# Optimization experiments

Hardware: AMD Instinct MI355X
Metric: run time of the kernel (lower is better)

## Reference

```python
import jax, jax.numpy as jnp
import numpy as np
from functools import partial

DIM = 1024
LIGHT_HID = 512   # dim * 0.5
HEAVY_HID = 4096  # dim * 4
NUM_HEAVY = 1024
N_ITERS = 50
K_ROUTE = 8.0
EPS = 0.1


def rms_norm(x, gamma):
    # F.normalize(x, dim=-1) * sqrt(dim) * gamma
    norm = jnp.linalg.norm(x, axis=-1, keepdims=True)
    normed = x / jnp.maximum(norm, 1e-12)
    return normed * (x.shape[-1] ** 0.5) * gamma


def ffn(x, gamma, w1, b1, w2, b2):
    h = rms_norm(x, gamma)
    h = jax.nn.gelu(h @ w1 + b1, approximate=False)
    return h @ w2 + b2


def coor_descent_route(x, routing_token, num_tokens):
    # s: [b, n]
    s = jnp.einsum('bnd,d->bn', x, routing_token)
    constant = EPS * jnp.log(jnp.asarray(K_ROUTE, dtype=s.dtype))
    b0 = -jax.nn.relu(s)
    a0 = jnp.zeros((s.shape[0], 1), dtype=s.dtype)

    def step(carry, _):
        a_prev, b = carry
        a = constant - EPS * jax.nn.logsumexp((s + b) / EPS, axis=-1, keepdims=True)
        b = -jax.nn.relu(s + a)
        return (a, b), None

    (a, b), _ = jax.lax.scan(step, (a0, b0), None, length=N_ITERS)
    scores = jnp.exp((s + a + b) / EPS)
    sel_scores, sel_idx = jax.lax.top_k(scores, num_tokens)
    # straight-through: value -> 1.0, gradient -> d(sel_scores)
    sel_scores = sel_scores + jax.lax.stop_gradient(1.0 - sel_scores)
    return sel_scores, sel_idx


def setup_inputs() -> dict:
    key = jax.random.key(0)
    ks = jax.random.split(key, 12)
    def lin(k, fan_in, fan_out):
        lim = 1.0 / np.sqrt(fan_in)
        kw, kb = jax.random.split(k)
        w = jax.random.uniform(kw, (fan_in, fan_out), jnp.float32, -lim, lim)
        b = jax.random.uniform(kb, (fan_out,), jnp.float32, -lim, lim)
        return w, b
    x = jax.random.normal(ks[0], (4, 8192, DIM), jnp.float32)
    routing_token = jax.random.normal(ks[1], (DIM,), jnp.float32)
    gamma_light = jnp.ones((DIM,), jnp.float32)
    w1_l, b1_l = lin(ks[2], DIM, LIGHT_HID)
    w2_l, b2_l = lin(ks[3], LIGHT_HID, DIM)
    gamma_heavy = jnp.ones((DIM,), jnp.float32)
    w1_h, b1_h = lin(ks[4], DIM, HEAVY_HID)
    w2_h, b2_h = lin(ks[5], HEAVY_HID, DIM)
    return dict(x=x, routing_token=routing_token,
                gamma_light=gamma_light, w1_light=w1_l, b1_light=b1_l,
                w2_light=w2_l, b2_light=b2_l,
                gamma_heavy=gamma_heavy, w1_heavy=w1_h, b1_heavy=b1_h,
                w2_heavy=w2_h, b2_heavy=b2_h)


def reference(x, routing_token, gamma_light, w1_light, b1_light, w2_light, b2_light,
              gamma_heavy, w1_heavy, b1_heavy, w2_heavy, b2_heavy):
    bsz = x.shape[0]
    light_out = ffn(x, gamma_light, w1_light, b1_light, w2_light, b2_light)
    sel_scores, sel_idx = coor_descent_route(x, routing_token, NUM_HEAVY)
    batch_range = jnp.arange(bsz)[:, None]           # [b, 1]
    routed = x[batch_range, sel_idx]                 # [b, k, d]
    routed_out = ffn(routed, gamma_heavy, w1_heavy, b1_heavy, w2_heavy, b2_heavy)
    routed_out = routed_out * sel_scores[..., None]
    heavy_out = jnp.zeros_like(x).at[batch_range, sel_idx].set(routed_out)
    return light_out + heavy_out
```

## Files before the change

### kernel.cpp

```cpp
#include <hip/hip_runtime.h>
#include <math.h>

#define TOKS   32768
#define NSEQ   8192
#define BATCH  4
#define DIMD   1024
#define LHID   512
#define HHID   4096
#define NHEAVY 1024

typedef __attribute__((ext_vector_type(8))) short bf16x8;
typedef __attribute__((ext_vector_type(4))) float f32x4;
typedef __attribute__((ext_vector_type(8))) unsigned short u16x8;
typedef __attribute__((ext_vector_type(4))) unsigned short u16x4;

__device__ __forceinline__ unsigned short bf16rne(float f) {
    unsigned u = __float_as_uint(f);
    return (unsigned short)((u + 0x7FFFu + ((u >> 16) & 1u)) >> 16);
}
__device__ __forceinline__ float gelu_f(float v) {
    return 0.5f * v * (1.0f + erff(v * 0.7071067811865476f));
}
__device__ __forceinline__ void gload_lds16(const unsigned short* g, unsigned short* l) {
#if defined(__HIP_DEVICE_COMPILE__)
    __builtin_amdgcn_global_load_lds((const __attribute__((address_space(1))) void*)g,
                                     (__attribute__((address_space(3))) void*)l,
                                     16, 0, 0);
#endif
}

__global__ __launch_bounds__(256) void k_rowscale(const float* __restrict__ x,
                                                  const float* __restrict__ rt,
                                                  const float* __restrict__ gamma,
                                                  float* __restrict__ s,
                                                  float* __restrict__ invr,
                                                  unsigned short* __restrict__ xl) {
    int wid = threadIdx.x >> 6, lane = threadIdx.x & 63;
    int row = blockIdx.x * 4 + wid;
    const float4* xr  = (const float4*)(x + (size_t)row * DIMD);
    const float4* rt4 = (const float4*)rt;
    const float4* g4  = (const float4*)gamma;
    float4 v[4];
    float dot = 0.f, ss = 0.f;
#pragma unroll
    for (int i = 0; i < 4; i++) {
        v[i] = xr[lane + 64 * i];
        float4 r = rt4[lane + 64 * i];
        dot += v[i].x * r.x + v[i].y * r.y + v[i].z * r.z + v[i].w * r.w;
        ss  += v[i].x * v[i].x + v[i].y * v[i].y + v[i].z * v[i].z + v[i].w * v[i].w;
    }
#pragma unroll
    for (int o = 32; o > 0; o >>= 1) {
        dot += __shfl_xor(dot, o);
        ss  += __shfl_xor(ss, o);
    }
    float iv = 32.0f / fmaxf(sqrtf(ss), 1e-12f);
    if (lane == 0) { s[row] = dot; invr[row] = iv; }
#pragma unroll
    for (int i = 0; i < 4; i++) {
        float4 g = g4[lane + 64 * i];
        u16x4 o;
        o[0] = bf16rne(v[i].x * iv * g.x);
        o[1] = bf16rne(v[i].y * iv * g.y);
        o[2] = bf16rne(v[i].z * iv * g.z);
        o[3] = bf16rne(v[i].w * iv * g.w);
        *(u16x4*)(xl + (size_t)row * DIMD + (lane + 64 * i) * 4) = o;
    }
}

__global__ __launch_bounds__(256) void k_rowstats(const float* __restrict__ x,
                                                  const float* __restrict__ rt,
                                                  float* __restrict__ s,
                                                  float* __restrict__ invr) {
    int wid = threadIdx.x >> 6, lane = threadIdx.x & 63;
    int row = blockIdx.x * 4 + wid;
    const float4* xr  = (const float4*)(x + (size_t)row * DIMD);
    const float4* rt4 = (const float4*)rt;
    float dot = 0.f, ss = 0.f;
#pragma unroll
    for (int i = 0; i < 4; i++) {
        float4 v = xr[lane + 64 * i];
        float4 r = rt4[lane + 64 * i];
        dot += v.x * r.x + v.y * r.y + v.z * r.z + v.w * r.w;
        ss  += v.x * v.x + v.y * v.y + v.z * v.z + v.w * v.w;
    }
#pragma unroll
    for (int o = 32; o > 0; o >>= 1) {
        dot += __shfl_down(dot, o);
        ss  += __shfl_down(ss, o);
    }
    if (lane == 0) {
        s[row] = dot;
        invr[row] = 32.0f / fmaxf(sqrtf(ss), 1e-12f);
    }
}

__global__ __launch_bounds__(1024) void k_routesel(const float* __restrict__ s_g,
                                                   int* __restrict__ rowmap) {
    int b = blockIdx.x, tid = threadIdx.x;
    int lane = tid & 63, wid = tid >> 6;
    __shared__ float red[2][16];
    __shared__ int wsum[16];
    __shared__ int ws2[16];
    __shared__ int PC[2];
    __shared__ int slot;
    __shared__ unsigned long long kk_[NSEQ];
    const float* sb = s_g + b * NSEQ;
    float sv[8];
    float smax = -3.4e38f;
#pragma unroll
    for (int i = 0; i < 8; i++) { sv[i] = sb[tid + 1024 * i]; smax = fmaxf(smax, sv[i]); }
#pragma unroll
    for (int o = 32; o > 0; o >>= 1) smax = fmaxf(smax, __shfl_xor(smax, o));
    if (lane == 0) red[0][wid] = smax;
    __syncthreads();
    float smaxAll = -3.4e38f;
    for (int w = 0; w < 16; w++) smaxAll = fmaxf(smaxAll, red[0][w]);
    __syncthreads();

    const float cst = 0.1f * logf(8.0f);
    float a = 0.0f;
    for (int it = 0; it < 50; it++) {
        float tau = -a;
        float M = fminf(smaxAll, tau);
        float p = 0.0f;
#pragma unroll
        for (int i = 0; i < 8; i++) p += expf((fminf(sv[i], tau) - M) * 10.0f);
#pragma unroll
        for (int o = 32; o > 0; o >>= 1) p += __shfl_xor(p, o);
        if (lane == 0) red[it & 1][wid] = p;
        __syncthreads();
        float S = 0.0f;
        for (int w = 0; w < 16; w++) S += red[it & 1][w];
        a = cst - M - 0.1f * logf(S);
        __syncthreads();
    }
    float sc[8];
    int p = 0, c1 = 0;
#pragma unroll
    for (int i = 0; i < 8; i++) {
        sc[i] = expf(fminf(sv[i] + a, 0.0f) * 10.0f);
        p  += (sc[i] > 0.0f) ? 1 : 0;
        c1 += (sc[i] == 1.0f) ? 1 : 0;
    }
    {
        int pp = p, cc = c1;
#pragma unroll
        for (int o = 32; o > 0; o >>= 1) {
            pp += __shfl_xor(pp, o);
            cc += __shfl_xor(cc, o);
        }
        if (lane == 0) { wsum[wid] = pp; ws2[wid] = cc; }
        __syncthreads();
        if (tid == 0) {
            int sp = 0, sC = 0;
            for (int w = 0; w < 16; w++) { sp += wsum[w]; sC += ws2[w]; }
            PC[0] = sp; PC[1] = sC;
        }
        __syncthreads();
    }
    int P = PC[0], C1 = PC[1];
    __syncthreads();

    if (C1 >= NHEAVY) {
        __shared__ unsigned char fl[NSEQ];
#pragma unroll
        for (int i = 0; i < 8; i++) fl[tid + 1024 * i] = (sc[i] == 1.0f) ? 1 : 0;
        __syncthreads();
        int zc = 0;
        unsigned char f[8];
#pragma unroll
        for (int j = 0; j < 8; j++) { f[j] = fl[tid * 8 + j]; zc += f[j]; }
        int inc = zc;
        for (int o = 1; o < 64; o <<= 1) {
            int t = __shfl_up(inc, o);
            if (lane >= o) inc += t;
        }
        if (lane == 63) wsum[wid] = inc;
        __syncthreads();
        if (tid == 0) {
            int acc = 0;
            for (int w = 0; w < 16; w++) { int t = wsum[w]; wsum[w] = acc; acc += t; }
        }
        __syncthreads();
        int rank = wsum[wid] + (inc - zc);
#pragma unroll
        for (int j = 0; j < 8; j++) {
            if (f[j]) {
                if (rank < NHEAVY) rowmap[b * NHEAVY + rank] = b * NSEQ + tid * 8 + j;
                rank++;
            }
        }
    } else if (P <= NHEAVY) {
        __shared__ unsigned char fl[NSEQ];
#pragma unroll
        for (int i = 0; i < 8; i++) fl[tid + 1024 * i] = (sc[i] > 0.0f) ? 1 : 0;
        __syncthreads();
        unsigned char pos[8]; int zc = 0;
#pragma unroll
        for (int j = 0; j < 8; j++) { pos[j] = fl[tid * 8 + j]; zc += pos[j] ? 0 : 1; }
        int inc = zc;
        for (int o = 1; o < 64; o <<= 1) {
            int t = __shfl_up(inc, o);
            if (lane >= o) inc += t;
        }
        if (lane == 63) wsum[wid] = inc;
        if (tid == 0) slot = 0;
        __syncthreads();
        if (tid == 0) {
            int acc = 0;
            for (int w = 0; w < 16; w++) { int t = wsum[w]; wsum[w] = acc; acc += t; }
        }
        __syncthreads();
        int zr = wsum[wid] + (inc - zc);
        int Z = NHEAVY - P;
#pragma unroll
        for (int j = 0; j < 8; j++) {
            int n = tid * 8 + j;
            bool sel;
            if (pos[j]) sel = true;
            else { sel = (zr < Z); zr += 1; }
            if (sel) {
                int sl = atomicAdd(&slot, 1);
                rowmap[b * NHEAVY + sl] = b * NSEQ + n;
            }
        }
    } else {
#pragma unroll
        for (int i = 0; i < 8; i++) {
            int n = tid + 1024 * i;
            kk_[n] = ((unsigned long long)__float_as_uint(sc[i]) << 32)
                   | (unsigned long long)(0xFFFFFFFFu - (unsigned)n);
        }
        __syncthreads();
        for (int k = 2; k <= NSEQ; k <<= 1) {
            for (int j = k >> 1; j > 0; j >>= 1) {
                for (int i = tid; i < NSEQ; i += 1024) {
                    int ixj = i ^ j;
                    if (ixj > i) {
                        unsigned long long u = kk_[i], v = kk_[ixj];
                        bool dirDesc = ((i & k) == 0);
                        if (dirDesc ? (u < v) : (u > v)) { kk_[i] = v; kk_[ixj] = u; }
                    }
                }
                __syncthreads();
            }
        }
        if (tid < NHEAVY) {
            unsigned idx = 0xFFFFFFFFu - (unsigned)(kk_[tid] & 0xFFFFFFFFull);
            rowmap[b * NHEAVY + tid] = b * NSEQ + (int)idx;
        }
    }
}

__global__ __launch_bounds__(1024) void k_route(const float* __restrict__ s_g,
                                                unsigned long long* __restrict__ keys,
                                                int* __restrict__ pcount,
                                                int* __restrict__ c1cnt) {
    int b = blockIdx.x, tid = threadIdx.x;
    int lane = tid & 63, wid = tid >> 6;
    const float* sb = s_g + b * NSEQ;
    float sv[8];
    float smax = -3.4e38f;
#pragma unroll
    for (int i = 0; i < 8; i++) { sv[i] = sb[tid + 1024 * i]; smax = fmaxf(smax, sv[i]); }
    __shared__ float red[2][16];
#pragma unroll
    for (int o = 32; o > 0; o >>= 1) smax = fmaxf(smax, __shfl_xor(smax, o));
    if (lane == 0) red[0][wid] = smax;
    __syncthreads();
    float smaxAll = -3.4e38f;
    for (int w = 0; w < 16; w++) smaxAll = fmaxf(smaxAll, red[0][w]);
    __syncthreads();
    const float cst = 0.1f * logf(8.0f);
    float a = 0.0f;
    for (int it = 0; it < 50; it++) {
        float tau = -a;
        float M = fminf(smaxAll, tau);
        float p = 0.0f;
#pragma unroll
        for (int i = 0; i < 8; i++) p += expf((fminf(sv[i], tau) - M) * 10.0f);
#pragma unroll
        for (int o = 32; o > 0; o >>= 1) p += __shfl_xor(p, o);
        if (lane == 0) red[it & 1][wid] = p;
        __syncthreads();
        float S = 0.0f;
        for (int w = 0; w < 16; w++) S += red[it & 1][w];
        a = cst - M - 0.1f * logf(S);
    }
    int p = 0, c1 = 0;
#pragma unroll
    for (int i = 0; i < 8; i++) {
        float sc = expf(fminf(sv[i] + a, 0.0f) * 10.0f);
        int n = tid + 1024 * i;
        keys[b * NSEQ + n] = ((unsigned long long)__float_as_uint(sc) << 32)
                           | (unsigned long long)(0xFFFFFFFFu - (unsigned)n);
        p  += (sc > 0.0f) ? 1 : 0;
        c1 += (sc == 1.0f) ? 1 : 0;
    }
#pragma unroll
    for (int o = 32; o > 0; o >>= 1) {
        p  += __shfl_xor(p, o);
        c1 += __shfl_xor(c1, o);
    }
    if (lane == 0) { atomicAdd(&pcount[b], p); atomicAdd(&c1cnt[b], c1); }
}

__global__ __launch_bounds__(1024) void k_select(const unsigned long long* __restrict__ keys,
                                                 const int* __restrict__ pcount,
                                                 const int* __restrict__ c1cnt,
                                                 int* __restrict__ rowmap) {
    int b = blockIdx.x, tid = threadIdx.x;
    int lane = tid & 63, wid = tid >> 6;
    __shared__ int wsum[16];
    __shared__ int slot;
    __shared__ unsigned long long kk_[NSEQ];
    int P = pcount[b], C1 = c1cnt[b];
    if (C1 >= NHEAVY) {
        bool f[8]; int zc = 0;
#pragma unroll
        for (int j = 0; j < 8; j++) {
            unsigned hi = (unsigned)(keys[b * NSEQ + tid * 8 + j] >> 32);
            f[j] = (hi == 0x3F800000u);
            zc += f[j] ? 1 : 0;
        }
        int inc = zc;
        for (int o = 1; o < 64; o <<= 1) {
            int t = __shfl_up(inc, o);
            if (lane >= o) inc += t;
        }
        if (lane == 63) wsum[wid] = inc;
        __syncthreads();
        if (tid == 0) {
            int acc = 0;
            for (int w = 0; w < 16; w++) { int t = wsum[w]; wsum[w] = acc; acc += t; }
        }
        __syncthreads();
        int rank = wsum[wid] + (inc - zc);
#pragma unroll
        for (int j = 0; j < 8; j++) {
            if (f[j]) {
                if (rank < NHEAVY) rowmap[b * NHEAVY + rank] = b * NSEQ + tid * 8 + j;
                rank++;
            }
        }
    } else if (P <= NHEAVY) {
        bool pos[8]; int zc = 0;
#pragma unroll
        for (int j = 0; j < 8; j++) {
            unsigned sbits = (unsigned)(keys[b * NSEQ + tid * 8 + j] >> 32);
            pos[j] = (sbits != 0u);
            zc += pos[j] ? 0 : 1;
        }
        int inc = zc;
        for (int o = 1; o < 64; o <<= 1) {
            int t = __shfl_up(inc, o);
            if (lane >= o) inc += t;
        }
        if (lane == 63) wsum[wid] = inc;
        if (tid == 0) slot = 0;
        __syncthreads();
        if (tid == 0) {
            int acc = 0;
            for (int w = 0; w < 16; w++) { int t = wsum[w]; wsum[w] = acc; acc += t; }
        }
        __syncthreads();
        int zr = wsum[wid] + (inc - zc);
        int Z = NHEAVY - P;
#pragma unroll
        for (int j = 0; j < 8; j++) {
            int n = tid * 8 + j;
            bool sel;
            if (pos[j]) sel = true;
            else { sel = (zr < Z); zr += 1; }
            if (sel) {
                int sl = atomicAdd(&slot, 1);
                rowmap[b * NHEAVY + sl] = b * NSEQ + n;
            }
        }
    } else {
        for (int i = tid; i < NSEQ; i += 1024) kk_[i] = keys[b * NSEQ + i];
        __syncthreads();
        for (int k = 2; k <= NSEQ; k <<= 1) {
            for (int j = k >> 1; j > 0; j >>= 1) {
                for (int i = tid; i < NSEQ; i += 1024) {
                    int ixj = i ^ j;
                    if (ixj > i) {
                        unsigned long long u = kk_[i], v = kk_[ixj];
                        bool dirDesc = ((i & k) == 0);
                        if (dirDesc ? (u < v) : (u > v)) { kk_[i] = v; kk_[ixj] = u; }
                    }
                }
                __syncthreads();
            }
        }
        unsigned idx = 0xFFFFFFFFu - (unsigned)(kk_[tid] & 0xFFFFFFFFull);
        rowmap[b * NHEAVY + tid] = b * NSEQ + (int)idx;
    }
}

__device__ __forceinline__ void transpose_body(const float* W, unsigned short* WT,
                                               int K, int N, int n0, int k0) {
    __shared__ float ts[64][65];
    int t = threadIdx.x;
    int kk = t >> 2, nc = (t & 3) * 16;
    const float4* src = (const float4*)(W + (size_t)(k0 + kk) * N + n0 + nc);
#pragma unroll
    for (int j = 0; j < 4; j++) {
        float4 v = src[j];
        ts[kk][nc + 4 * j + 0] = v.x;
        ts[kk][nc + 4 * j + 1] = v.y;
        ts[kk][nc + 4 * j + 2] = v.z;
        ts[kk][nc + 4 * j + 3] = v.w;
    }
    __syncthreads();
    int nn = t >> 2, kc = (t & 3) * 16;
    unsigned short o[16];
#pragma unroll
    for (int j = 0; j < 16; j++) o[j] = bf16rne(ts[kc + j][nn]);
    unsigned short* dst = WT + (size_t)(n0 + nn) * K + k0 + kc;
    *(u16x8*)(dst)     = *(u16x8*)(o);
    *(u16x8*)(dst + 8) = *(u16x8*)(o + 8);
}

__global__ __launch_bounds__(256) void k_transpose(const float* __restrict__ W,
                                                   unsigned short* __restrict__ WT,
                                                   int K, int N) {
    transpose_body(W, WT, K, N, blockIdx.x * 64, blockIdx.y * 64);
}

__global__ __launch_bounds__(256) void k_transpose4(
        const float* w1l, unsigned short* w1lT,
        const float* w2l, unsigned short* w2lT,
        const float* w1h, unsigned short* w1hT,
        const float* w2h, unsigned short* w2hT) {
    int w = (int)blockIdx.x;
    if (w < 128)       { int i = w;        transpose_body(w1l, w1lT, DIMD, LHID, (i % 8) * 64,  (i / 8) * 64); }
    else if (w < 256)  { int i = w - 128;  transpose_body(w2l, w2lT, LHID, DIMD, (i % 16) * 64, (i / 16) * 64); }
    else if (w < 1280) { int i = w - 256;  transpose_body(w1h, w1hT, DIMD, HHID, (i % 64) * 64, (i / 64) * 64); }
    else               { int i = w - 1280; transpose_body(w2h, w2hT, HHID, DIMD, (i % 16) * 64, (i / 16) * 64); }
}

__global__ __launch_bounds__(256) void k_prescale(const float* __restrict__ x,
                                                  const float* __restrict__ invr,
                                                  const float* __restrict__ gamma,
                                                  const int* __restrict__ rowmap,
                                                  unsigned short* __restrict__ xo,
                                                  int row_ofs) {
    int t = threadIdx.x;
    int i = blockIdx.x * 2 + (t >> 7);
    int c = (t & 127) * 8;
    int src = rowmap ? rowmap[i] : (row_ofs + i);
    float iv = invr[src];
    const float4* px = (const float4*)(x + (size_t)src * DIMD + c);
    const float4* pg = (const float4*)(gamma + c);
    float4 v0 = px[0], v1 = px[1];
    float4 g0 = pg[0], g1 = pg[1];
    unsigned short o[8];
    o[0] = bf16rne(v0.x * iv * g0.x); o[1] = bf16rne(v0.y * iv * g0.y);
    o[2] = bf16rne(v0.z * iv * g0.z); o[3] = bf16rne(v0.w * iv * g0.w);
    o[4] = bf16rne(v1.x * iv * g1.x); o[5] = bf16rne(v1.y * iv * g1.y);
    o[6] = bf16rne(v1.z * iv * g1.z); o[7] = bf16rne(v1.w * iv * g1.w);
    *(u16x8*)(xo + (size_t)i * DIMD + c) = *(u16x8*)o;
}

__global__ __launch_bounds__(256) void k_scatter(const float* __restrict__ rb,
                                                 const int* __restrict__ rowmap,
                                                 float* __restrict__ out) {
    int i = blockIdx.x;
    int c = threadIdx.x * 4;
    int g = rowmap[i];
    float4 v = *(const float4*)(rb + (size_t)i * DIMD + c);
    float* p = out + (size_t)g * DIMD + c;
    float4 o = *(const float4*)p;
    o.x += v.x; o.y += v.y; o.z += v.z; o.w += v.w;
    *(float4*)p = o;
}

struct GArg {
    const unsigned short* A; const unsigned short* BT; const float* bias;
    void* C; const int* rowmap;
    int K, kslice, m_ofs, ldc, nx, ny;
};

template<int EPI>
__device__ __forceinline__ void gemm_body(const GArg ga, int w, int nwg,
                                          unsigned short* As, unsigned short* Bs) {
    int tid = threadIdx.x;
    int q = nwg >> 3, r = nwg & 7;
    int xcd = w & 7, sub = w >> 3;
    int id = (xcd < r ? xcd * (q + 1) : r * (q + 1) + (xcd - r) * q) + sub;
    int bx = id % ga.nx;
    int t2 = id / ga.nx;
    int by = t2 % ga.ny;
    int bz = t2 / ga.ny;

    int m0 = by * 128, n0 = bx * 128;
    int kbeg = bz * ga.kslice, kend = kbeg + ga.kslice;
    int K = ga.K;
    int lane = tid & 63, wid = tid >> 6;
    int wm = wid >> 1, wn = wid & 1;
    int lc = lane & 15, lr = lane >> 4;

    int srow = lane >> 3;
    int sslot = (lane & 7) ^ srow;
    const unsigned short* paA = ga.A  + (size_t)(m0 + srow) * K + sslot * 8;
    const unsigned short* paB = ga.BT + (size_t)(n0 + srow) * K + sslot * 8;

    f32x4 acc[4][4];
#pragma unroll
    for (int i = 0; i < 4; i++)
#pragma unroll
        for (int j = 0; j < 4; j++) acc[i][j] = (f32x4){0.f, 0.f, 0.f, 0.f};

    for (int k0 = kbeg; k0 < kend; k0 += 64) {
        if (k0 != kbeg) __syncthreads();
#pragma unroll
        for (int qq = 0; qq < 4; qq++) {
            int rb_ = (wid * 4 + qq) * 8;
            gload_lds16(paA + (size_t)rb_ * K + k0, &As[rb_ * 64]);
            gload_lds16(paB + (size_t)rb_ * K + k0, &Bs[rb_ * 64]);
        }
        __syncthreads();
#pragma unroll
        for (int ks = 0; ks < 2; ks++) {
            bf16x8 af[4], bfr[4];
#pragma unroll
            for (int f = 0; f < 4; f++) {
                int rowA = wm * 64 + f * 16 + lc;
                int rowB = wn * 64 + f * 16 + lc;
                int sw = ((ks * 4 + lr) ^ (lc & 7)) << 4;
                af[f]  = *(const bf16x8*)((const char*)As + rowA * 128 + sw);
                bfr[f] = *(const bf16x8*)((const char*)Bs + rowB * 128 + sw);
            }
#pragma unroll
            for (int fm = 0; fm < 4; fm++)
#pragma unroll
                for (int fn = 0; fn < 4; fn++)
                    acc[fm][fn] = __builtin_amdgcn_mfma_f32_16x16x32_bf16(
                        af[fm], bfr[fn], acc[fm][fn], 0, 0, 0);
        }
    }

    float bcol[4];
#pragma unroll
    for (int fn = 0; fn < 4; fn++) {
        float bb = ga.bias[n0 + wn * 64 + fn * 16 + lc];
        if constexpr (EPI == 3) { if (bz != 0) bb = 0.0f; }
        bcol[fn] = bb;
    }
#pragma unroll
    for (int fm = 0; fm < 4; fm++) {
        int rowb = m0 + wm * 64 + fm * 16 + lr * 4;
#pragma unroll
        for (int fn = 0; fn < 4; fn++) {
            int col = n0 + wn * 64 + fn * 16 + lc;
            f32x4 v = acc[fm][fn];
#pragma unroll
            for (int rr = 0; rr < 4; rr++) {
                float val = v[rr] + bcol[fn];
                if constexpr (EPI == 0) {
                    ((unsigned short*)ga.C)[(size_t)(rowb + rr) * ga.ldc + col] =
                        bf16rne(gelu_f(val));
                } else if constexpr (EPI == 1) {
                    ((float*)ga.C)[(size_t)(ga.m_ofs + rowb + rr) * ga.ldc + col] = val;
                } else if constexpr (EPI == 2) {
                    int g = ga.rowmap[ga.m_ofs + rowb + rr];
                    float* p = (float*)ga.C + (size_t)g * ga.ldc + col;
                    *p = *p + val;
                } else {
                    int g = ga.rowmap ? ga.rowmap[rowb + rr] : (rowb + rr);
                    atomicAdd((float*)ga.C + (size_t)g * ga.ldc + col, val);
                }
            }
        }
    }
}

template<int EPI>
__global__ __launch_bounds__(256, 4) void k_mfma(GArg ga) {
    __shared__ unsigned short sm[2][128 * 64];
    gemm_body<EPI>(ga, (int)blockIdx.x, (int)gridDim.x, sm[0], sm[1]);
}

template<int EA, int EB>
__global__ __launch_bounds__(256, 4) void k_mfma2(GArg a, GArg b, int nwgA) {
    __shared__ unsigned short sm[2][128 * 64];
    int w = (int)blockIdx.x;
    if (w < nwgA) gemm_body<EA>(a, w, nwgA, sm[0], sm[1]);
    else          gemm_body<EB>(b, w - nwgA, (int)gridDim.x - nwgA, sm[0], sm[1]);
}

extern "C" void kernel_launch(void* const* d_in, const int* in_sizes, int n_in,
                              void* d_out, int out_size, void* d_ws, size_t ws_size,
                              hipStream_t stream) {
    const float* x   = (const float*)d_in[0];
    const float* rt  = (const float*)d_in[1];
    const float* gl  = (const float*)d_in[2];
    const float* w1l = (const float*)d_in[3];
    const float* b1l = (const float*)d_in[4];
    const float* w2l = (const float*)d_in[5];
    const float* b2l = (const float*)d_in[6];
    const float* gh  = (const float*)d_in[7];
    const float* w1h = (const float*)d_in[8];
    const float* b1h = (const float*)d_in[9];
    const float* w2h = (const float*)d_in[10];
    const float* b2h = (const float*)d_in[11];
    float* out = (float*)d_out;

    char* ws = (char*)d_ws;
    float* s    = (float*)(ws);
    float* invr = (float*)(ws + 131072);
    unsigned long long* keys = (unsigned long long*)(ws + 262144);
    int* rowmap = (int*)(ws + 524288);
    int* pcount = (int*)(ws + 540672);
    int* c1cnt  = pcount + 4;
    size_t off = 1u << 20;
    unsigned short* w1lT = (unsigned short*)(ws + off); off += (size_t)LHID * DIMD * 2;
    unsigned short* w2lT = (unsigned short*)(ws + off); off += (size_t)DIMD * LHID * 2;
    unsigned short* w1hT = (unsigned short*)(ws + off); off += (size_t)HHID * DIMD * 2;
    unsigned short* w2hT = (unsigned short*)(ws + off); off += (size_t)DIMD * HHID * 2;
    unsigned short* xhg  = (unsigned short*)(ws + off); off += (size_t)BATCH * NHEAVY * DIMD * 2;
    char* un = ws + off;
    size_t U = ws_size > off ? ws_size - off : 0;

    const size_t XL_B = (size_t)TOKS * DIMD * 2;
    const size_t HL_B = (size_t)TOKS * LHID * 2;
    const size_t HH_B = (size_t)BATCH * NHEAVY * HHID * 2;
    bool big = (U >= XL_B + HL_B + HH_B);

    const long MH = (long)BATCH * NHEAVY;

    if (big) {
        unsigned short* xl = (unsigned short*)un;
        unsigned short* hl = (unsigned short*)(un + XL_B);
        unsigned short* hh = (unsigned short*)(un + XL_B + HL_B);
        float* rb = (float*)un;

        k_rowscale<<<TOKS / 4, 256, 0, stream>>>(x, rt, gl, s, invr, xl);
        k_routesel<<<BATCH, 1024, 0, stream>>>(s, rowmap);
        k_transpose4<<<2304, 256, 0, stream>>>(w1l, w1lT, w2l, w2lT, w1h, w1hT, w2h, w2hT);
        k_prescale<<<(unsigned)(MH / 2), 256, 0, stream>>>(x, invr, gh, rowmap, xhg, 0);

        GArg hg1{xhg, w1hT, b1h, hh, nullptr, DIMD, DIMD, 0, HHID, HHID / 128, (int)MH / 128};
        GArg lg1{xl,  w1lT, b1l, hl, nullptr, DIMD, DIMD, 0, LHID, LHID / 128, TOKS / 128};
        k_mfma2<0, 0><<<2048, 256, 0, stream>>>(hg1, lg1, 1024);

        GArg hg2{hh, w2hT, b2h, rb,  nullptr, HHID, HHID, 0, DIMD, DIMD / 128, (int)MH / 128};
        GArg lg2{hl, w2lT, b2l, out, nullptr, LHID, LHID, 0, DIMD, DIMD / 128, TOKS / 128};
        k_mfma2<1, 1><<<2304, 256, 0, stream>>>(hg2, lg2, 256);

        k_scatter<<<(unsigned)MH, 256, 0, stream>>>(rb, rowmap, out);
    } else {
        hipMemsetAsync(pcount, 0, 32, stream);
        k_rowstats<<<TOKS / 4, 256, 0, stream>>>(x, rt, s, invr);
        k_route<<<BATCH, 1024, 0, stream>>>(s, keys, pcount, c1cnt);
        k_select<<<BATCH, 1024, 0, stream>>>(keys, pcount, c1cnt, rowmap);

        k_transpose<<<dim3(LHID / 64, DIMD / 64), 256, 0, stream>>>(w1l, w1lT, DIMD, LHID);
        k_transpose<<<dim3(DIMD / 64, LHID / 64), 256, 0, stream>>>(w2l, w2lT, LHID, DIMD);
        k_transpose<<<dim3(HHID / 64, DIMD / 64), 256, 0, stream>>>(w1h, w1hT, DIMD, HHID);
        k_transpose<<<dim3(DIMD / 64, HHID / 64), 256, 0, stream>>>(w2h, w2hT, HHID, DIMD);

        long Rl = (long)(U / 3072);
        Rl -= Rl % 128; if (Rl < 128) Rl = 128; if (Rl > TOKS) Rl = TOKS;
        unsigned short* xl = (unsigned short*)un;
        unsigned short* hl = (unsigned short*)(un + (size_t)Rl * DIMD * 2);
        for (long mo = 0; mo < TOKS; mo += Rl) {
            long R = TOKS - mo < Rl ? TOKS - mo : Rl;
            k_prescale<<<(unsigned)(R / 2), 256, 0, stream>>>(x, invr, gl, nullptr, xl, (int)mo);
            GArg a1{xl, w1lT, b1l, hl, nullptr, DIMD, DIMD, 0, LHID, LHID / 128, (int)(R / 128)};
            k_mfma<0><<<(LHID / 128) * (unsigned)(R / 128), 256, 0, stream>>>(a1);
            GArg a2{hl, w2lT, b2l, out, nullptr, LHID, LHID, (int)mo, DIMD, DIMD / 128, (int)(R / 128)};
            k_mfma<1><<<(DIMD / 128) * (unsigned)(R / 128), 256, 0, stream>>>(a2);
        }

        k_prescale<<<(unsigned)(MH / 2), 256, 0, stream>>>(x, invr, gh, rowmap, xhg, 0);
        long Rh = (long)(U / ((size_t)HHID * 2));
        Rh -= Rh % 128; if (Rh < 128) Rh = 128; if (Rh > MH) Rh = MH;
        unsigned short* hh = (unsigned short*)un;
        for (long mo = 0; mo < MH; mo += Rh) {
            long R = MH - mo < Rh ? MH - mo : Rh;
            GArg b1{xhg + (size_t)mo * DIMD, w1hT, b1h, hh, nullptr, DIMD, DIMD, 0, HHID,
                    HHID / 128, (int)(R / 128)};
            k_mfma<0><<<(HHID / 128) * (unsigned)(R / 128), 256, 0, stream>>>(b1);
            GArg b2{hh, w2hT, b2h, out, rowmap, HHID, HHID, (int)mo, DIMD,
                    DIMD / 128, (int)(R / 128)};
            k_mfma<2><<<(DIMD / 128) * (unsigned)(R / 128), 256, 0, stream>>>(b2);
        }
    }
}
```

Measured before the change: 358.2 us.

## Fold gamma into weights, apply row norm in GEMM epilogue, gather heavy rows directly

The row-stats pass now writes x as plain bf16 without normalization, and gamma is folded into the transposed W1 weights. The per-row inverse norm is applied in the first GEMM epilogue (EPI 5 and 6). The heavy GEMM gathers its A rows through rowmap straight from the shared bf16 copy, which removes the separate prescale kernel. The transpose work is merged into the same pre-kernel launch, dropping launches and one pass over the heavy inputs. The cost is extra indirect loads in the heavy GEMM and slightly different bf16 rounding, since normalization now happens after quantization.

```diff
diff --git a/kernel.cpp b/kernel.cpp
--- a/kernel.cpp
+++ b/kernel.cpp
@@ -29,42 +29,80 @@
 #endif
 }
 
-__global__ __launch_bounds__(256) void k_rowscale(const float* __restrict__ x,
-                                                  const float* __restrict__ rt,
-                                                  const float* __restrict__ gamma,
-                                                  float* __restrict__ s,
-                                                  float* __restrict__ invr,
-                                                  unsigned short* __restrict__ xl) {
-    int wid = threadIdx.x >> 6, lane = threadIdx.x & 63;
-    int row = blockIdx.x * 4 + wid;
-    const float4* xr  = (const float4*)(x + (size_t)row * DIMD);
-    const float4* rt4 = (const float4*)rt;
-    const float4* g4  = (const float4*)gamma;
-    float4 v[4];
-    float dot = 0.f, ss = 0.f;
-#pragma unroll
-    for (int i = 0; i < 4; i++) {
-        v[i] = xr[lane + 64 * i];
-        float4 r = rt4[lane + 64 * i];
-        dot += v[i].x * r.x + v[i].y * r.y + v[i].z * r.z + v[i].w * r.w;
-        ss  += v[i].x * v[i].x + v[i].y * v[i].y + v[i].z * v[i].z + v[i].w * v[i].w;
-    }
-#pragma unroll
-    for (int o = 32; o > 0; o >>= 1) {
-        dot += __shfl_xor(dot, o);
-        ss  += __shfl_xor(ss, o);
-    }
-    float iv = 32.0f / fmaxf(sqrtf(ss), 1e-12f);
-    if (lane == 0) { s[row] = dot; invr[row] = iv; }
-#pragma unroll
-    for (int i = 0; i < 4; i++) {
-        float4 g = g4[lane + 64 * i];
-        u16x4 o;
-        o[0] = bf16rne(v[i].x * iv * g.x);
-        o[1] = bf16rne(v[i].y * iv * g.y);
-        o[2] = bf16rne(v[i].z * iv * g.z);
-        o[3] = bf16rne(v[i].w * iv * g.w);
-        *(u16x4*)(xl + (size_t)row * DIMD + (lane + 64 * i) * 4) = o;
+__device__ __forceinline__ void transpose_body(const float* W, unsigned short* WT,
+                                               int K, int N, int n0, int k0,
+                                               const float* grow) {
+    __shared__ float ts[64][65];
+    int t = threadIdx.x;
+    int kk = t >> 2, nc = (t & 3) * 16;
+    float gs = grow ? grow[k0 + kk] : 1.0f;
+    const float4* src = (const float4*)(W + (size_t)(k0 + kk) * N + n0 + nc);
+#pragma unroll
+    for (int j = 0; j < 4; j++) {
+        float4 v = src[j];
+        ts[kk][nc + 4 * j + 0] = v.x * gs;
+        ts[kk][nc + 4 * j + 1] = v.y * gs;
+        ts[kk][nc + 4 * j + 2] = v.z * gs;
+        ts[kk][nc + 4 * j + 3] = v.w * gs;
+    }
+    __syncthreads();
+    int nn = t >> 2, kc = (t & 3) * 16;
+    unsigned short o[16];
+#pragma unroll
+    for (int j = 0; j < 16; j++) o[j] = bf16rne(ts[kc + j][nn]);
+    unsigned short* dst = WT + (size_t)(n0 + nn) * K + k0 + kc;
+    *(u16x8*)(dst)     = *(u16x8*)(o);
+    *(u16x8*)(dst + 8) = *(u16x8*)(o + 8);
+}
+
+__global__ __launch_bounds__(256) void k_pre(const float* __restrict__ x,
+                                             const float* __restrict__ rt,
+                                             const float* __restrict__ gl,
+                                             const float* __restrict__ gh,
+                                             const float* w1l, unsigned short* w1lT,
+                                             const float* w2l, unsigned short* w2lT,
+                                             const float* w1h, unsigned short* w1hT,
+                                             const float* w2h, unsigned short* w2hT,
+                                             float* __restrict__ s,
+                                             float* __restrict__ invr,
+                                             unsigned short* __restrict__ xc) {
+    int b = (int)blockIdx.x;
+    if (b < 8192) {
+        int wid = threadIdx.x >> 6, lane = threadIdx.x & 63;
+        int row = b * 4 + wid;
+        const float4* xr  = (const float4*)(x + (size_t)row * DIMD);
+        const float4* rt4 = (const float4*)rt;
+        float4 v[4];
+        float dot = 0.f, ss = 0.f;
+#pragma unroll
+        for (int i = 0; i < 4; i++) {
+            v[i] = xr[lane + 64 * i];
+            float4 r = rt4[lane + 64 * i];
+            dot += v[i].x * r.x + v[i].y * r.y + v[i].z * r.z + v[i].w * r.w;
+            ss  += v[i].x * v[i].x + v[i].y * v[i].y + v[i].z * v[i].z + v[i].w * v[i].w;
+        }
+#pragma unroll
+        for (int o = 32; o > 0; o >>= 1) {
+            dot += __shfl_xor(dot, o);
+            ss  += __shfl_xor(ss, o);
+        }
+        if (lane == 0) {
+            s[row] = dot;
+            invr[row] = 32.0f / fmaxf(sqrtf(ss), 1e-12f);
+        }
+#pragma unroll
+        for (int i = 0; i < 4; i++) {
+            u16x4 o;
+            o[0] = bf16rne(v[i].x); o[1] = bf16rne(v[i].y);
+            o[2] = bf16rne(v[i].z); o[3] = bf16rne(v[i].w);
+            *(u16x4*)(xc + (size_t)row * DIMD + (lane + 64 * i) * 4) = o;
+        }
+    } else {
+        int w = b - 8192;
+        if (w < 128)       { int i = w;        transpose_body(w1l, w1lT, DIMD, LHID, (i % 8) * 64,  (i / 8) * 64, gl); }
+        else if (w < 256)  { int i = w - 128;  transpose_body(w2l, w2lT, LHID, DIMD, (i % 16) * 64, (i / 16) * 64, nullptr); }
+        else if (w < 1280) { int i = w - 256;  transpose_body(w1h, w1hT, DIMD, HHID, (i % 64) * 64, (i / 64) * 64, gh); }
+        else               { int i = w - 1280; transpose_body(w2h, w2hT, HHID, DIMD, (i % 16) * 64, (i / 16) * 64, nullptr); }
     }
 }
 
@@ -399,46 +437,10 @@
     }
 }
 
-__device__ __forceinline__ void transpose_body(const float* W, unsigned short* WT,
-                                               int K, int N, int n0, int k0) {
-    __shared__ float ts[64][65];
-    int t = threadIdx.x;
-    int kk = t >> 2, nc = (t & 3) * 16;
-    const float4* src = (const float4*)(W + (size_t)(k0 + kk) * N + n0 + nc);
-#pragma unroll
-    for (int j = 0; j < 4; j++) {
-        float4 v = src[j];
-        ts[kk][nc + 4 * j + 0] = v.x;
-        ts[kk][nc + 4 * j + 1] = v.y;
-        ts[kk][nc + 4 * j + 2] = v.z;
-        ts[kk][nc + 4 * j + 3] = v.w;
-    }
-    __syncthreads();
-    int nn = t >> 2, kc = (t & 3) * 16;
-    unsigned short o[16];
-#pragma unroll
-    for (int j = 0; j < 16; j++) o[j] = bf16rne(ts[kc + j][nn]);
-    unsigned short* dst = WT + (size_t)(n0 + nn) * K + k0 + kc;
-    *(u16x8*)(dst)     = *(u16x8*)(o);
-    *(u16x8*)(dst + 8) = *(u16x8*)(o + 8);
-}
-
 __global__ __launch_bounds__(256) void k_transpose(const float* __restrict__ W,
                                                    unsigned short* __restrict__ WT,
                                                    int K, int N) {
-    transpose_body(W, WT, K, N, blockIdx.x * 64, blockIdx.y * 64);
-}
-
-__global__ __launch_bounds__(256) void k_transpose4(
-        const float* w1l, unsigned short* w1lT,
-        const float* w2l, unsigned short* w2lT,
-        const float* w1h, unsigned short* w1hT,
-        const float* w2h, unsigned short* w2hT) {
-    int w = (int)blockIdx.x;
-    if (w < 128)       { int i = w;        transpose_body(w1l, w1lT, DIMD, LHID, (i % 8) * 64,  (i / 8) * 64); }
-    else if (w < 256)  { int i = w - 128;  transpose_body(w2l, w2lT, LHID, DIMD, (i % 16) * 64, (i / 16) * 64); }
-    else if (w < 1280) { int i = w - 256;  transpose_body(w1h, w1hT, DIMD, HHID, (i % 64) * 64, (i / 64) * 64); }
-    else               { int i = w - 1280; transpose_body(w2h, w2hT, HHID, DIMD, (i % 16) * 64, (i / 16) * 64); }
+    transpose_body(W, WT, K, N, blockIdx.x * 64, blockIdx.y * 64, nullptr);
 }
 
 __global__ __launch_bounds__(256) void k_prescale(const float* __restrict__ x,
@@ -479,7 +481,7 @@
 
 struct GArg {
     const unsigned short* A; const unsigned short* BT; const float* bias;
-    void* C; const int* rowmap;
+    void* C; const int* rowmap; const float* invr;
     int K, kslice, m_ofs, ldc, nx, ny;
 };
 
@@ -494,6 +496,7 @@
     int t2 = id / ga.nx;
     int by = t2 % ga.ny;
     int bz = t2 / ga.ny;
+    (void)bz;
 
     int m0 = by * 128, n0 = bx * 128;
     int kbeg = bz * ga.kslice, kend = kbeg + ga.kslice;
@@ -504,8 +507,17 @@
 
     int srow = lane >> 3;
     int sslot = (lane & 7) ^ srow;
-    const unsigned short* paA = ga.A  + (size_t)(m0 + srow) * K + sslot * 8;
     const unsigned short* paB = ga.BT + (size_t)(n0 + srow) * K + sslot * 8;
+    const unsigned short* paA;
+    int growq[4];
+    if constexpr (EPI == 6) {
+#pragma unroll
+        for (int qq = 0; qq < 4; qq++)
+            growq[qq] = ga.rowmap[m0 + (wid * 4 + qq) * 8 + srow];
+        paA = ga.A + sslot * 8;
+    } else {
+        paA = ga.A + (size_t)(m0 + srow) * K + sslot * 8;
+    }
 
     f32x4 acc[4][4];
 #pragma unroll
@@ -518,7 +530,10 @@
 #pragma unroll
         for (int qq = 0; qq < 4; qq++) {
             int rb_ = (wid * 4 + qq) * 8;
-            gload_lds16(paA + (size_t)rb_ * K + k0, &As[rb_ * 64]);
+            if constexpr (EPI == 6)
+                gload_lds16(paA + (size_t)growq[qq] * K + k0, &As[rb_ * 64]);
+            else
+                gload_lds16(paA + (size_t)rb_ * K + k0, &As[rb_ * 64]);
             gload_lds16(paB + (size_t)rb_ * K + k0, &Bs[rb_ * 64]);
         }
         __syncthreads();
@@ -544,11 +559,7 @@
 
     float bcol[4];
 #pragma unroll
-    for (int fn = 0; fn < 4; fn++) {
-        float bb = ga.bias[n0 + wn * 64 + fn * 16 + lc];
-        if constexpr (EPI == 3) { if (bz != 0) bb = 0.0f; }
-        bcol[fn] = bb;
-    }
+    for (int fn = 0; fn < 4; fn++) bcol[fn] = ga.bias[n0 + wn * 64 + fn * 16 + lc];
 #pragma unroll
     for (int fm = 0; fm < 4; fm++) {
         int rowb = m0 + wm * 64 + fm * 16 + lr * 4;
@@ -558,19 +569,26 @@
             f32x4 v = acc[fm][fn];
 #pragma unroll
             for (int rr = 0; rr < 4; rr++) {
-                float val = v[rr] + bcol[fn];
                 if constexpr (EPI == 0) {
+                    float val = v[rr] + bcol[fn];
                     ((unsigned short*)ga.C)[(size_t)(rowb + rr) * ga.ldc + col] =
                         bf16rne(gelu_f(val));
                 } else if constexpr (EPI == 1) {
-                    ((float*)ga.C)[(size_t)(ga.m_ofs + rowb + rr) * ga.ldc + col] = val;
+                    ((float*)ga.C)[(size_t)(ga.m_ofs + rowb + rr) * ga.ldc + col] =
+                        v[rr] + bcol[fn];
                 } else if constexpr (EPI == 2) {
                     int g = ga.rowmap[ga.m_ofs + rowb + rr];
                     float* p = (float*)ga.C + (size_t)g * ga.ldc + col;
-                    *p = *p + val;
+                    *p = *p + v[rr] + bcol[fn];
+                } else if constexpr (EPI == 5) {
+                    float val = v[rr] * ga.invr[rowb + rr] + bcol[fn];
+                    ((unsigned short*)ga.C)[(size_t)(rowb + rr) * ga.ldc + col] =
+                        bf16rne(gelu_f(val));
                 } else {
-                    int g = ga.rowmap ? ga.rowmap[rowb + rr] : (rowb + rr);
-                    atomicAdd((float*)ga.C + (size_t)g * ga.ldc + col, val);
+                    int g = ga.rowmap[rowb + rr];
+                    float val = v[rr] * ga.invr[g] + bcol[fn];
+                    ((unsigned short*)ga.C)[(size_t)(rowb + rr) * ga.ldc + col] =
+                        bf16rne(gelu_f(val));
                 }
             }
         }
@@ -632,22 +650,23 @@
     const long MH = (long)BATCH * NHEAVY;
 
     if (big) {
-        unsigned short* xl = (unsigned short*)un;
+        unsigned short* xc = (unsigned short*)un;
         unsigned short* hl = (unsigned short*)(un + XL_B);
         unsigned short* hh = (unsigned short*)(un + XL_B + HL_B);
         float* rb = (float*)un;
 
-        k_rowscale<<<TOKS / 4, 256, 0, stream>>>(x, rt, gl, s, invr, xl);
+        k_pre<<<8192 + 2304, 256, 0, stream>>>(x, rt, gl, gh,
+                                               w1l, w1lT, w2l, w2lT,
+                                               w1h, w1hT, w2h, w2hT,
+                                               s, invr, xc);
         k_routesel<<<BATCH, 1024, 0, stream>>>(s, rowmap);
-        k_transpose4<<<2304, 256, 0, stream>>>(w1l, w1lT, w2l, w2lT, w1h, w1hT, w2h, w2hT);
-        k_prescale<<<(unsigned)(MH / 2), 256, 0, stream>>>(x, invr, gh, rowmap, xhg, 0);
-
-        GArg hg1{xhg, w1hT, b1h, hh, nullptr, DIMD, DIMD, 0, HHID, HHID / 128, (int)MH / 128};
-        GArg lg1{xl,  w1lT, b1l, hl, nullptr, DIMD, DIMD, 0, LHID, LHID / 128, TOKS / 128};
-        k_mfma2<0, 0><<<2048, 256, 0, stream>>>(hg1, lg1, 1024);
-
-        GArg hg2{hh, w2hT, b2h, rb,  nullptr, HHID, HHID, 0, DIMD, DIMD / 128, (int)MH / 128};
-        GArg lg2{hl, w2lT, b2l, out, nullptr, LHID, LHID, 0, DIMD, DIMD / 128, TOKS / 128};
+
+        GArg hg1{xc, w1hT, b1h, hh, rowmap, invr, DIMD, DIMD, 0, HHID, HHID / 128, (int)MH / 128};
+        GArg lg1{xc, w1lT, b1l, hl, nullptr, invr, DIMD, DIMD, 0, LHID, LHID / 128, TOKS / 128};
+        k_mfma2<6, 5><<<2048, 256, 0, stream>>>(hg1, lg1, 1024);
+
+        GArg hg2{hh, w2hT, b2h, rb,  nullptr, nullptr, HHID, HHID, 0, DIMD, DIMD / 128, (int)MH / 128};
+        GArg lg2{hl, w2lT, b2l, out, nullptr, nullptr, LHID, LHID, 0, DIMD, DIMD / 128, TOKS / 128};
         k_mfma2<1, 1><<<2304, 256, 0, stream>>>(hg2, lg2, 256);
 
         k_scatter<<<(unsigned)MH, 256, 0, stream>>>(rb, rowmap, out);
@@ -669,9 +688,9 @@
         for (long mo = 0; mo < TOKS; mo += Rl) {
             long R = TOKS - mo < Rl ? TOKS - mo : Rl;
             k_prescale<<<(unsigned)(R / 2), 256, 0, stream>>>(x, invr, gl, nullptr, xl, (int)mo);
-            GArg a1{xl, w1lT, b1l, hl, nullptr, DIMD, DIMD, 0, LHID, LHID / 128, (int)(R / 128)};
+            GArg a1{xl, w1lT, b1l, hl, nullptr, nullptr, DIMD, DIMD, 0, LHID, LHID / 128, (int)(R / 128)};
             k_mfma<0><<<(LHID / 128) * (unsigned)(R / 128), 256, 0, stream>>>(a1);
-            GArg a2{hl, w2lT, b2l, out, nullptr, LHID, LHID, (int)mo, DIMD, DIMD / 128, (int)(R / 128)};
+            GArg a2{hl, w2lT, b2l, out, nullptr, nullptr, LHID, LHID, (int)mo, DIMD, DIMD / 128, (int)(R / 128)};
             k_mfma<1><<<(DIMD / 128) * (unsigned)(R / 128), 256, 0, stream>>>(a2);
         }
 
@@ -681,10 +700,10 @@
         unsigned short* hh = (unsigned short*)un;
         for (long mo = 0; mo < MH; mo += Rh) {
             long R = MH - mo < Rh ? MH - mo : Rh;
-            GArg b1{xhg + (size_t)mo * DIMD, w1hT, b1h, hh, nullptr, DIMD, DIMD, 0, HHID,
+            GArg b1{xhg + (size_t)mo * DIMD, w1hT, b1h, hh, nullptr, nullptr, DIMD, DIMD, 0, HHID,
                     HHID / 128, (int)(R / 128)};
             k_mfma<0><<<(HHID / 128) * (unsigned)(R / 128), 256, 0, stream>>>(b1);
-            GArg b2{hh, w2hT, b2h, out, rowmap, HHID, HHID, (int)mo, DIMD,
+            GArg b2{hh, w2hT, b2h, out, rowmap, nullptr, HHID, HHID, (int)mo, DIMD,
                     DIMD / 128, (int)(R / 128)};
             k_mfma<2><<<(DIMD / 128) * (unsigned)(R / 128), 256, 0, stream>>>(b2);
         }
```

Result: faster. 333.2 us (median of 3 runs) (-7.0%).
